# Kernel optimization log

Measured on AMD Instinct MI355X. Metric: run time of the kernel, lower is better.

Reference implementation:

```python
import jax, jax.numpy as jnp
import numpy as np

D_MODEL = 1024
NUM_HEADS = 16
D_K = D_MODEL // NUM_HEADS
LN_EPS = 1e-5


def setup_inputs() -> dict:
    key = jax.random.key(0)
    ks = jax.random.split(key, 13)
    B, S, D = 2, 2048, D_MODEL
    s = 1.0 / np.sqrt(D)
    return {
        "query": jax.random.normal(ks[0], (B, S, D), jnp.float32),
        "key": jax.random.normal(ks[1], (B, S, D), jnp.float32),
        "value": jax.random.normal(ks[2], (B, S, D), jnp.float32),
        "Wq": jax.random.normal(ks[3], (D, D), jnp.float32) * s,
        "bq": jnp.zeros((D,), jnp.float32),
        "Wk": jax.random.normal(ks[4], (D, D), jnp.float32) * s,
        "bk": jnp.zeros((D,), jnp.float32),
        "Wv": jax.random.normal(ks[5], (D, D), jnp.float32) * s,
        "bv": jnp.zeros((D,), jnp.float32),
        "Wo": jax.random.normal(ks[6], (D, D), jnp.float32) * s,
        "bo": jnp.zeros((D,), jnp.float32),
        "gamma": jnp.ones((D,), jnp.float32),
        "beta": jnp.zeros((D,), jnp.float32),
    }


def _mha(query, key, value, Wq, bq, Wk, bk, Wv, bv, Wo, bo, gamma, beta):
    B, S, D = query.shape
    H, dk = NUM_HEADS, D_K
    # projections (x @ W + b), reshape to [B, H, S, dk]
    Q = (query @ Wq + bq).reshape(B, S, H, dk).transpose(0, 2, 1, 3)
    K = (key @ Wk + bk).reshape(B, S, H, dk).transpose(0, 2, 1, 3)
    V = (value @ Wv + bv).reshape(B, S, H, dk).transpose(0, 2, 1, 3)
    scores = jnp.einsum("bhsd,bhtd->bhst", Q, K) / np.sqrt(dk).astype(np.float32)
    attn = jax.nn.softmax(scores, axis=-1)  # dropout is identity at inference
    ctx = jnp.einsum("bhst,bhtd->bhsd", attn, V)
    ctx = ctx.transpose(0, 2, 1, 3).reshape(B, S, D)
    out = ctx @ Wo + bo
    # residual + LayerNorm
    x = out + query
    mu = jnp.mean(x, axis=-1, keepdims=True)
    var = jnp.mean(jnp.square(x - mu), axis=-1, keepdims=True)
    y = (x - mu) / jnp.sqrt(var + LN_EPS) * gamma + beta
    return y, attn


def reference(query, key, value, Wq, bq, Wk, bk, Wv, bv, Wo, bo, gamma, beta):
    return _mha(query, key, value, Wq, bq, Wk, bk, Wv, bv, Wo, bo, gamma, beta)
```

## Files before the change

kernel.cpp:

```cpp
#include <hip/hip_runtime.h>
#include <stdint.h>

typedef __attribute__((ext_vector_type(8))) short bf16x8;
typedef __attribute__((ext_vector_type(4))) float f32x4;
typedef unsigned short u16;

#define DEVINL static __device__ __forceinline__

namespace {
constexpr int kS = 2048, kD = 1024, kH = 16, kDK = 64;
constexpr int kBS = 4096, kBH = 32;
constexpr float kEps = 1e-5f;
constexpr float kQScale = 0.125f * 1.44269504088896340736f;
}

DEVINL u16 f2bf(float f) {
  union { float f; unsigned u; } v; v.f = f;
  unsigned r = v.u + 0x7fffu + ((v.u >> 16) & 1u);
  return (u16)(r >> 16);
}
DEVINL unsigned pk2(float lo, float hi) {
  return (__float_as_uint(hi) & 0xffff0000u) | (__float_as_uint(lo) >> 16);
}
DEVINL f32x4 mfma16(bf16x8 a, bf16x8 b, f32x4 c) {
  return __builtin_amdgcn_mfma_f32_16x16x32_bf16(a, b, c, 0, 0, 0);
}

__global__ __launch_bounds__(256, 4)
void k_cvt_x(const float* __restrict__ xq, const float* __restrict__ xk,
             const float* __restrict__ xv, u16* __restrict__ oq,
             u16* __restrict__ ok, u16* __restrict__ ov) {
  const int z = blockIdx.y;
  const float* __restrict__ src = (z == 0) ? xq : (z == 1) ? xk : xv;
  u16* __restrict__ dst = (z == 0) ? oq : (z == 1) ? ok : ov;
  const size_t idx = (size_t)blockIdx.x * 256 + threadIdx.x;
  const float4 a = *reinterpret_cast<const float4*>(&src[idx * 8]);
  const float4 b = *reinterpret_cast<const float4*>(&src[idx * 8 + 4]);
  uint4 o;
  o.x = pk2(a.x, a.y); o.y = pk2(a.z, a.w);
  o.z = pk2(b.x, b.y); o.w = pk2(b.z, b.w);
  *reinterpret_cast<uint4*>(&dst[idx * 8]) = o;
}

__global__ __launch_bounds__(256, 4)
void k_cvt_w(const float* __restrict__ wq, const float* __restrict__ wk,
             const float* __restrict__ wv, const float* __restrict__ wo,
             u16* __restrict__ oq, u16* __restrict__ ok,
             u16* __restrict__ ov, u16* __restrict__ oo) {
  const int z = blockIdx.z;
  const float* __restrict__ W = (z == 0) ? wq : (z == 1) ? wk : (z == 2) ? wv : wo;
  u16* __restrict__ Wt = (z == 0) ? oq : (z == 1) ? ok : (z == 2) ? ov : oo;
  const int n0 = blockIdx.x * 64, k0 = blockIdx.y * 64;
  const int tid = threadIdx.x;
  __shared__ u16 Tl[64][65];
#pragma unroll
  for (int p = 0; p < 4; ++p) {
    const int idx = tid + p * 256;
    const int kr = idx >> 4, cg = (idx & 15) * 4;
    const float4 v = *reinterpret_cast<const float4*>(&W[(size_t)(k0 + kr) * kD + n0 + cg]);
    Tl[kr][cg + 0] = f2bf(v.x);
    Tl[kr][cg + 1] = f2bf(v.y);
    Tl[kr][cg + 2] = f2bf(v.z);
    Tl[kr][cg + 3] = f2bf(v.w);
  }
  __syncthreads();
  const int n = tid >> 2, kc = (tid & 3) * 16;
  u16 buf[16];
#pragma unroll
  for (int i = 0; i < 16; ++i) buf[i] = Tl[kc + i][n];
  *reinterpret_cast<bf16x8*>(&Wt[(size_t)(n0 + n) * kD + k0 + kc]) =
      *reinterpret_cast<const bf16x8*>(&buf[0]);
  *reinterpret_cast<bf16x8*>(&Wt[(size_t)(n0 + n) * kD + k0 + kc + 8]) =
      *reinterpret_cast<const bf16x8*>(&buf[8]);
}

__global__ __launch_bounds__(256, 2)
void k_proj(const u16* __restrict__ Xq, const u16* __restrict__ Xk,
            const u16* __restrict__ Xv, const u16* __restrict__ Wtq,
            const u16* __restrict__ Wtk, const u16* __restrict__ Wtv,
            const float* __restrict__ bq, const float* __restrict__ bk,
            const float* __restrict__ bv, u16* __restrict__ Qo,
            u16* __restrict__ Ko, u16* __restrict__ Vo) {
  const int which = blockIdx.z;
  const u16* __restrict__ X = (which == 0) ? Xq : (which == 1) ? Xk : Xv;
  const u16* __restrict__ Wt = (which == 0) ? Wtq : (which == 1) ? Wtk : Wtv;
  const float* __restrict__ bias = (which == 0) ? bq : (which == 1) ? bk : bv;

  const int n0 = blockIdx.x * 128, m0 = blockIdx.y * 128;
  const int tid = threadIdx.x, w = tid >> 6, l = tid & 63;
  const int l15 = l & 15, lh = l >> 4;

  __shared__ u16 Al[128][72];
  __shared__ u16 Bl[128][72];

  f32x4 acc[2][8];
#pragma unroll
  for (int i = 0; i < 2; ++i)
#pragma unroll
    for (int j = 0; j < 8; ++j) acc[i][j] = f32x4{0.f, 0.f, 0.f, 0.f};

  for (int k0 = 0; k0 < kD; k0 += 64) {
    __syncthreads();
#pragma unroll
    for (int p = 0; p < 4; ++p) {
      const int idx = tid + p * 256;
      const int row = idx >> 3, c = (idx & 7) * 8;
      *reinterpret_cast<bf16x8*>(&Al[row][c]) =
          *reinterpret_cast<const bf16x8*>(&X[(size_t)(m0 + row) * kD + k0 + c]);
      *reinterpret_cast<bf16x8*>(&Bl[row][c]) =
          *reinterpret_cast<const bf16x8*>(&Wt[(size_t)(n0 + row) * kD + k0 + c]);
    }
    __syncthreads();
#pragma unroll
    for (int kq = 0; kq < 2; ++kq) {
      const int kk = kq * 32 + lh * 8;
      bf16x8 a[2], b[8];
#pragma unroll
      for (int mi = 0; mi < 2; ++mi)
        a[mi] = *reinterpret_cast<const bf16x8*>(&Al[w * 32 + mi * 16 + l15][kk]);
#pragma unroll
      for (int nj = 0; nj < 8; ++nj)
        b[nj] = *reinterpret_cast<const bf16x8*>(&Bl[nj * 16 + l15][kk]);
      if (which == 2) {
#pragma unroll
        for (int mi = 0; mi < 2; ++mi)
#pragma unroll
          for (int nj = 0; nj < 8; ++nj)
            acc[mi][nj] = mfma16(a[mi], b[nj], acc[mi][nj]);
      } else {
#pragma unroll
        for (int mi = 0; mi < 2; ++mi)
#pragma unroll
          for (int nj = 0; nj < 8; ++nj)
            acc[mi][nj] = mfma16(b[nj], a[mi], acc[mi][nj]);
      }
    }
  }

  if (which == 2) {
#pragma unroll
    for (int mi = 0; mi < 2; ++mi)
#pragma unroll
      for (int nj = 0; nj < 8; ++nj) {
        const int col = n0 + nj * 16 + l15;
        const int h = col >> 6, d = col & 63;
        const float bvv = bias[col];
        const int row0 = m0 + w * 32 + mi * 16 + lh * 4;
        const int b_ = row0 >> 11, s0 = row0 & 2047;
        uint2 pkv;
        pkv.x = pk2(acc[mi][nj][0] + bvv, acc[mi][nj][1] + bvv);
        pkv.y = pk2(acc[mi][nj][2] + bvv, acc[mi][nj][3] + bvv);
        *reinterpret_cast<uint2*>(
            &Vo[((size_t)(b_ * kH + h) * kDK + d) * kS + s0]) = pkv;
      }
  } else {
    u16* __restrict__ Out = (which == 0) ? Qo : Ko;
    const float os = (which == 0) ? kQScale : 1.0f;
#pragma unroll
    for (int mi = 0; mi < 2; ++mi) {
      const int srow = m0 + w * 32 + mi * 16 + l15;
      const int b_ = srow >> 11, s_ = srow & 2047;
#pragma unroll
      for (int nj = 0; nj < 8; ++nj) {
        const int c0 = n0 + nj * 16 + lh * 4;
        const int h = c0 >> 6, d0 = c0 & 63;
        const float4 b4 = *reinterpret_cast<const float4*>(&bias[c0]);
        uint2 pkv;
        pkv.x = pk2((acc[mi][nj][0] + b4.x) * os, (acc[mi][nj][1] + b4.y) * os);
        pkv.y = pk2((acc[mi][nj][2] + b4.z) * os, (acc[mi][nj][3] + b4.w) * os);
        *reinterpret_cast<uint2*>(
            &Out[((size_t)(b_ * kH + h) * kS + s_) * kDK + d0]) = pkv;
      }
    }
  }
}

__global__ __launch_bounds__(256, 2)
void k_attn(const u16* __restrict__ Qw, const u16* __restrict__ Kw,
            const u16* __restrict__ Vtw, float* __restrict__ attn_out,
            u16* __restrict__ ctx_out) {
  const int q0 = blockIdx.x * 128;
  const int bh = blockIdx.y;
  const int tid = threadIdx.x, w = tid >> 6, l = tid & 63;
  const int l15 = l & 15, lh = l >> 4;

  __shared__ u16 PQs[128][72];
  __shared__ u16 Ksh[2][64][72];
  __shared__ u16 Vsh[2][64][72];

  const u16* __restrict__ Qg = Qw + ((size_t)bh * kS + q0) * kDK;
  const u16* __restrict__ Kg = Kw + (size_t)bh * kS * kDK;
  const u16* __restrict__ Vtg = Vtw + (size_t)bh * kDK * kS;

#pragma unroll
  for (int p = 0; p < 4; ++p) {
    const int idx = tid + p * 256;
    const int row = idx >> 3, c = (idx & 7) * 8;
    *reinterpret_cast<bf16x8*>(&PQs[row][c]) =
        *reinterpret_cast<const bf16x8*>(&Qg[(size_t)row * kDK + c]);
  }
  bf16x8 kreg[2], vreg[2];
#pragma unroll
  for (int p = 0; p < 2; ++p) {
    const int idx = tid + p * 256;
    const int row = idx >> 3, c = (idx & 7) * 8;
    kreg[p] = *reinterpret_cast<const bf16x8*>(&Kg[(size_t)row * kDK + c]);
  }
#pragma unroll
  for (int p = 0; p < 2; ++p) {
    const int idx = tid + p * 256;
    const int row = idx >> 3, c = (idx & 7) * 8;
    *reinterpret_cast<bf16x8*>(&Ksh[0][row][c]) = kreg[p];
  }
  __syncthreads();

  bf16x8 qf[2][2];
#pragma unroll
  for (int mi = 0; mi < 2; ++mi)
#pragma unroll
    for (int kq = 0; kq < 2; ++kq)
      qf[mi][kq] = *reinterpret_cast<const bf16x8*>(
          &PQs[w * 32 + mi * 16 + l15][kq * 32 + lh * 8]);

  float lsum[2] = {0.f, 0.f};
  for (int t = 0; t < 32; ++t) {
    const int buf = t & 1;
    if (t + 1 < 32) {
      const u16* __restrict__ src = Kg + (size_t)(t + 1) * 64 * kDK;
#pragma unroll
      for (int p = 0; p < 2; ++p) {
        const int idx = tid + p * 256;
        const int row = idx >> 3, c = (idx & 7) * 8;
        kreg[p] = *reinterpret_cast<const bf16x8*>(&src[(size_t)row * kDK + c]);
      }
    }
    f32x4 sacc[2][4];
#pragma unroll
    for (int mi = 0; mi < 2; ++mi)
#pragma unroll
      for (int nj = 0; nj < 4; ++nj) sacc[mi][nj] = f32x4{0.f, 0.f, 0.f, 0.f};
    __builtin_amdgcn_s_setprio(1);
#pragma unroll
    for (int kq = 0; kq < 2; ++kq) {
      const int kk = kq * 32 + lh * 8;
      bf16x8 kf[4];
#pragma unroll
      for (int nj = 0; nj < 4; ++nj)
        kf[nj] = *reinterpret_cast<const bf16x8*>(&Ksh[buf][nj * 16 + l15][kk]);
#pragma unroll
      for (int mi = 0; mi < 2; ++mi)
#pragma unroll
        for (int nj = 0; nj < 4; ++nj)
          sacc[mi][nj] = mfma16(kf[nj], qf[mi][kq], sacc[mi][nj]);
    }
    __builtin_amdgcn_s_setprio(0);
#pragma unroll
    for (int mi = 0; mi < 2; ++mi) {
      float s0 = 0.f;
#pragma unroll
      for (int nj = 0; nj < 4; ++nj)
#pragma unroll
        for (int r = 0; r < 4; ++r) s0 += exp2f(sacc[mi][nj][r]);
      lsum[mi] += s0;
    }
    if (t + 1 < 32) {
#pragma unroll
      for (int p = 0; p < 2; ++p) {
        const int idx = tid + p * 256;
        const int row = idx >> 3, c = (idx & 7) * 8;
        *reinterpret_cast<bf16x8*>(&Ksh[buf ^ 1][row][c]) = kreg[p];
      }
    }
    __syncthreads();
  }

  float lg[2];
#pragma unroll
  for (int mi = 0; mi < 2; ++mi) {
    float lv = lsum[mi];
    lv += __shfl_xor(lv, 16, 64);
    lv += __shfl_xor(lv, 32, 64);
    lg[mi] = -log2f(lv);
  }

  f32x4 oacc[2][4];
#pragma unroll
  for (int mi = 0; mi < 2; ++mi)
#pragma unroll
    for (int ni = 0; ni < 4; ++ni) oacc[mi][ni] = f32x4{0.f, 0.f, 0.f, 0.f};

  float* __restrict__ attn_base =
      attn_out + (size_t)bh * kS * kS + (size_t)q0 * kS;

#pragma unroll
  for (int p = 0; p < 2; ++p) {
    const int idx = tid + p * 256;
    const int row = idx >> 3, c = (idx & 7) * 8;
    kreg[p] = *reinterpret_cast<const bf16x8*>(&Kg[(size_t)row * kDK + c]);
    vreg[p] = *reinterpret_cast<const bf16x8*>(&Vtg[(size_t)row * kS + c]);
  }
#pragma unroll
  for (int p = 0; p < 2; ++p) {
    const int idx = tid + p * 256;
    const int row = idx >> 3, c = (idx & 7) * 8;
    *reinterpret_cast<bf16x8*>(&Ksh[0][row][c]) = kreg[p];
    *reinterpret_cast<bf16x8*>(&Vsh[0][row][c]) = vreg[p];
  }
  __syncthreads();

  for (int t = 0; t < 32; ++t) {
    const int buf = t & 1;
    const int t0 = t * 64;
    if (t + 1 < 32) {
      const u16* __restrict__ ksrc = Kg + (size_t)(t0 + 64) * kDK;
#pragma unroll
      for (int p = 0; p < 2; ++p) {
        const int idx = tid + p * 256;
        const int row = idx >> 3, c = (idx & 7) * 8;
        kreg[p] = *reinterpret_cast<const bf16x8*>(&ksrc[(size_t)row * kDK + c]);
        vreg[p] = *reinterpret_cast<const bf16x8*>(&Vtg[(size_t)row * kS + t0 + 64 + c]);
      }
    }
    f32x4 sacc[2][4];
#pragma unroll
    for (int mi = 0; mi < 2; ++mi)
#pragma unroll
      for (int nj = 0; nj < 4; ++nj) sacc[mi][nj] = f32x4{0.f, 0.f, 0.f, 0.f};
    __builtin_amdgcn_s_setprio(1);
#pragma unroll
    for (int kq = 0; kq < 2; ++kq) {
      const int kk = kq * 32 + lh * 8;
      bf16x8 kf[4];
#pragma unroll
      for (int nj = 0; nj < 4; ++nj)
        kf[nj] = *reinterpret_cast<const bf16x8*>(&Ksh[buf][nj * 16 + l15][kk]);
#pragma unroll
      for (int mi = 0; mi < 2; ++mi)
#pragma unroll
        for (int nj = 0; nj < 4; ++nj)
          sacc[mi][nj] = mfma16(kf[nj], qf[mi][kq], sacc[mi][nj]);
    }
    __builtin_amdgcn_s_setprio(0);
#pragma unroll
    for (int mi = 0; mi < 2; ++mi) {
      const int q = w * 32 + mi * 16 + l15;
      float* __restrict__ arow = attn_base + (size_t)q * kS + t0;
#pragma unroll
      for (int nj = 0; nj < 4; ++nj) {
        float4 pv;
        pv.x = exp2f(sacc[mi][nj][0] + lg[mi]);
        pv.y = exp2f(sacc[mi][nj][1] + lg[mi]);
        pv.z = exp2f(sacc[mi][nj][2] + lg[mi]);
        pv.w = exp2f(sacc[mi][nj][3] + lg[mi]);
        *reinterpret_cast<float4*>(&arow[nj * 16 + lh * 4]) = pv;
        uint2 pkv; pkv.x = pk2(pv.x, pv.y); pkv.y = pk2(pv.z, pv.w);
        *reinterpret_cast<uint2*>(&PQs[q][nj * 16 + lh * 4]) = pkv;
      }
    }
    __builtin_amdgcn_s_setprio(1);
#pragma unroll
    for (int kq = 0; kq < 2; ++kq) {
      const int kk = kq * 32 + lh * 8;
      bf16x8 pa[2], vb[4];
#pragma unroll
      for (int mi = 0; mi < 2; ++mi)
        pa[mi] = *reinterpret_cast<const bf16x8*>(&PQs[w * 32 + mi * 16 + l15][kk]);
#pragma unroll
      for (int ni = 0; ni < 4; ++ni)
        vb[ni] = *reinterpret_cast<const bf16x8*>(&Vsh[buf][ni * 16 + l15][kk]);
#pragma unroll
      for (int mi = 0; mi < 2; ++mi)
#pragma unroll
        for (int ni = 0; ni < 4; ++ni)
          oacc[mi][ni] = mfma16(vb[ni], pa[mi], oacc[mi][ni]);
    }
    __builtin_amdgcn_s_setprio(0);
    if (t + 1 < 32) {
#pragma unroll
      for (int p = 0; p < 2; ++p) {
        const int idx = tid + p * 256;
        const int row = idx >> 3, c = (idx & 7) * 8;
        *reinterpret_cast<bf16x8*>(&Ksh[buf ^ 1][row][c]) = kreg[p];
        *reinterpret_cast<bf16x8*>(&Vsh[buf ^ 1][row][c]) = vreg[p];
      }
    }
    __syncthreads();
  }

  const int b_ = bh >> 4, h = bh & 15;
#pragma unroll
  for (int mi = 0; mi < 2; ++mi) {
    const int s_ = q0 + w * 32 + mi * 16 + l15;
#pragma unroll
    for (int ni = 0; ni < 4; ++ni) {
      const int d0 = ni * 16 + lh * 4;
      uint2 pkv;
      pkv.x = pk2(oacc[mi][ni][0], oacc[mi][ni][1]);
      pkv.y = pk2(oacc[mi][ni][2], oacc[mi][ni][3]);
      *reinterpret_cast<uint2*>(
          &ctx_out[((size_t)(b_ * kS + s_)) * kD + h * kDK + d0]) = pkv;
    }
  }
}

__global__ __launch_bounds__(256, 2)
void k_oproj(const u16* __restrict__ Cw, const u16* __restrict__ Wto,
             const float* __restrict__ bo, const float* __restrict__ query,
             float* __restrict__ Xout) {
  const int n0 = blockIdx.x * 128, m0 = blockIdx.y * 128;
  const int tid = threadIdx.x, w = tid >> 6, l = tid & 63;
  const int l15 = l & 15, lh = l >> 4;

  __shared__ u16 Al[128][72];
  __shared__ u16 Bl[128][72];

  f32x4 acc[2][8];
#pragma unroll
  for (int i = 0; i < 2; ++i)
#pragma unroll
    for (int j = 0; j < 8; ++j) acc[i][j] = f32x4{0.f, 0.f, 0.f, 0.f};

  for (int k0 = 0; k0 < kD; k0 += 64) {
    __syncthreads();
#pragma unroll
    for (int p = 0; p < 4; ++p) {
      const int idx = tid + p * 256;
      const int row = idx >> 3, c = (idx & 7) * 8;
      *reinterpret_cast<bf16x8*>(&Al[row][c]) =
          *reinterpret_cast<const bf16x8*>(&Cw[(size_t)(m0 + row) * kD + k0 + c]);
      *reinterpret_cast<bf16x8*>(&Bl[row][c]) =
          *reinterpret_cast<const bf16x8*>(&Wto[(size_t)(n0 + row) * kD + k0 + c]);
    }
    __syncthreads();
#pragma unroll
    for (int kq = 0; kq < 2; ++kq) {
      const int kk = kq * 32 + lh * 8;
      bf16x8 a[2], b[8];
#pragma unroll
      for (int mi = 0; mi < 2; ++mi)
        a[mi] = *reinterpret_cast<const bf16x8*>(&Al[w * 32 + mi * 16 + l15][kk]);
#pragma unroll
      for (int nj = 0; nj < 8; ++nj)
        b[nj] = *reinterpret_cast<const bf16x8*>(&Bl[nj * 16 + l15][kk]);
#pragma unroll
      for (int mi = 0; mi < 2; ++mi)
#pragma unroll
        for (int nj = 0; nj < 8; ++nj)
          acc[mi][nj] = mfma16(b[nj], a[mi], acc[mi][nj]);
    }
  }

#pragma unroll
  for (int mi = 0; mi < 2; ++mi) {
    const int row = m0 + w * 32 + mi * 16 + l15;
#pragma unroll
    for (int nj = 0; nj < 8; ++nj) {
      const int c0 = n0 + nj * 16 + lh * 4;
      const float4 b4 = *reinterpret_cast<const float4*>(&bo[c0]);
      const float4 q4 = *reinterpret_cast<const float4*>(&query[(size_t)row * kD + c0]);
      float4 o;
      o.x = acc[mi][nj][0] + b4.x + q4.x;
      o.y = acc[mi][nj][1] + b4.y + q4.y;
      o.z = acc[mi][nj][2] + b4.z + q4.z;
      o.w = acc[mi][nj][3] + b4.w + q4.w;
      *reinterpret_cast<float4*>(&Xout[(size_t)row * kD + c0]) = o;
    }
  }
}

__global__ __launch_bounds__(256, 4)
void k_ln(float* __restrict__ Y, const float* __restrict__ gamma,
          const float* __restrict__ beta) {
  const int row = blockIdx.x;
  float* __restrict__ x = Y + (size_t)row * kD;
  const int tid = threadIdx.x;
  const float4 v = reinterpret_cast<const float4*>(x)[tid];
  float s = v.x + v.y + v.z + v.w;
  float sq = v.x * v.x + v.y * v.y + v.z * v.z + v.w * v.w;
#pragma unroll
  for (int mk = 1; mk < 64; mk <<= 1) {
    s += __shfl_xor(s, mk, 64);
    sq += __shfl_xor(sq, mk, 64);
  }
  __shared__ float ss[4], ssq[4];
  if ((tid & 63) == 0) { ss[tid >> 6] = s; ssq[tid >> 6] = sq; }
  __syncthreads();
  s = ss[0] + ss[1] + ss[2] + ss[3];
  sq = ssq[0] + ssq[1] + ssq[2] + ssq[3];
  const float mu = s * (1.f / kD);
  const float rstd = rsqrtf(sq * (1.f / kD) - mu * mu + kEps);
  const float4 g = reinterpret_cast<const float4*>(gamma)[tid];
  const float4 bb = reinterpret_cast<const float4*>(beta)[tid];
  float4 o;
  o.x = (v.x - mu) * rstd * g.x + bb.x;
  o.y = (v.y - mu) * rstd * g.y + bb.y;
  o.z = (v.z - mu) * rstd * g.z + bb.z;
  o.w = (v.w - mu) * rstd * g.w + bb.w;
  reinterpret_cast<float4*>(x)[tid] = o;
}

extern "C" void kernel_launch(void* const* d_in, const int* in_sizes, int n_in,
                              void* d_out, int out_size, void* d_ws, size_t ws_size,
                              hipStream_t stream) {
  (void)in_sizes; (void)n_in; (void)out_size; (void)ws_size;
  const float* query = (const float*)d_in[0];
  const float* key_i = (const float*)d_in[1];
  const float* value = (const float*)d_in[2];
  const float* Wq = (const float*)d_in[3];
  const float* bq = (const float*)d_in[4];
  const float* Wk = (const float*)d_in[5];
  const float* bk = (const float*)d_in[6];
  const float* Wv = (const float*)d_in[7];
  const float* bv = (const float*)d_in[8];
  const float* Wo = (const float*)d_in[9];
  const float* bo = (const float*)d_in[10];
  const float* gamma = (const float*)d_in[11];
  const float* beta = (const float*)d_in[12];

  float* y_out = (float*)d_out;
  float* attn_out = y_out + (size_t)kBS * kD;

  u16* Xbq = (u16*)d_ws;
  u16* Xbk = Xbq + (size_t)kBS * kD;
  u16* Xbv = Xbk + (size_t)kBS * kD;
  u16* Wtq = Xbv + (size_t)kBS * kD;
  u16* Wtk = Wtq + (size_t)kD * kD;
  u16* Wtv = Wtk + (size_t)kD * kD;
  u16* Wto = Wtv + (size_t)kD * kD;
  u16* Qw  = Wto + (size_t)kD * kD;
  u16* Kw  = Qw + (size_t)kBH * kS * kDK;
  u16* Vtw = Kw + (size_t)kBH * kS * kDK;
  u16* Cw  = Xbq;

  k_cvt_x<<<dim3(2048, 3), 256, 0, stream>>>(query, key_i, value, Xbq, Xbk, Xbv);
  k_cvt_w<<<dim3(16, 16, 4), 256, 0, stream>>>(Wq, Wk, Wv, Wo, Wtq, Wtk, Wtv, Wto);
  k_proj<<<dim3(kD / 128, kBS / 128, 3), 256, 0, stream>>>(
      Xbq, Xbk, Xbv, Wtq, Wtk, Wtv, bq, bk, bv, Qw, Kw, Vtw);
  k_attn<<<dim3(kS / 128, kBH), 256, 0, stream>>>(Qw, Kw, Vtw, attn_out, Cw);
  k_oproj<<<dim3(kD / 128, kBS / 128), 256, 0, stream>>>(Cw, Wto, bo, query, y_out);
  k_ln<<<dim3(kBS), 256, 0, stream>>>(y_out, gamma, beta);
}
```

Before: 316.1 us.

## Load GEMM tiles directly to LDS with XOR-swizzled layout in projections

The QKV and output projection GEMMs now use global_load_lds (16-byte direct global-to-LDS copies) instead of staging tiles through registers. The LDS tiles drop their padding and use an XOR swizzle on 8-element k-chunks to avoid bank conflicts. Occupancy hints rise from 2 to 3 blocks per CU, which the smaller LDS footprint allows. This aims to cut register pressure and VGPR round trips during tile loads, but the correctness of the swizzle and the direct-to-LDS addressing depends on the per-wave LDS base layout.

```diff
diff --git a/kernel.cpp b/kernel.cpp
--- a/kernel.cpp
+++ b/kernel.cpp
@@ -25,6 +25,12 @@
 DEVINL f32x4 mfma16(bf16x8 a, bf16x8 b, f32x4 c) {
   return __builtin_amdgcn_mfma_f32_16x16x32_bf16(a, b, c, 0, 0, 0);
 }
+DEVINL void gl_lds16(const u16* g, u16* l) {
+  __builtin_amdgcn_global_load_lds(
+      (const __attribute__((address_space(1))) void*)(g),
+      (__attribute__((address_space(3))) void*)(l), 16, 0, 0);
+}
+DEVINL int kswz(int kq, int lh, int aswz) { return (((kq << 2) + lh) ^ aswz) << 3; }
 
 __global__ __launch_bounds__(256, 4)
 void k_cvt_x(const float* __restrict__ xq, const float* __restrict__ xk,
@@ -74,7 +80,7 @@
       *reinterpret_cast<const bf16x8*>(&buf[8]);
 }
 
-__global__ __launch_bounds__(256, 2)
+__global__ __launch_bounds__(256, 3)
 void k_proj(const u16* __restrict__ Xq, const u16* __restrict__ Xk,
             const u16* __restrict__ Xv, const u16* __restrict__ Wtq,
             const u16* __restrict__ Wtk, const u16* __restrict__ Wtv,
@@ -89,9 +95,10 @@
   const int n0 = blockIdx.x * 128, m0 = blockIdx.y * 128;
   const int tid = threadIdx.x, w = tid >> 6, l = tid & 63;
   const int l15 = l & 15, lh = l >> 4;
-
-  __shared__ u16 Al[128][72];
-  __shared__ u16 Bl[128][72];
+  const int aswz = l15 & 7;
+
+  __shared__ u16 Al[128][64];
+  __shared__ u16 Bl[128][64];
 
   f32x4 acc[2][8];
 #pragma unroll
@@ -103,17 +110,18 @@
     __syncthreads();
 #pragma unroll
     for (int p = 0; p < 4; ++p) {
-      const int idx = tid + p * 256;
-      const int row = idx >> 3, c = (idx & 7) * 8;
-      *reinterpret_cast<bf16x8*>(&Al[row][c]) =
-          *reinterpret_cast<const bf16x8*>(&X[(size_t)(m0 + row) * kD + k0 + c]);
-      *reinterpret_cast<bf16x8*>(&Bl[row][c]) =
-          *reinterpret_cast<const bf16x8*>(&Wt[(size_t)(n0 + row) * kD + k0 + c]);
+      const int slot = p * 256 + tid;
+      const int row = slot >> 3;
+      const int k8 = (slot & 7) ^ (row & 7);
+      gl_lds16(&X[(size_t)(m0 + row) * kD + k0 + k8 * 8],
+               &Al[0][0] + (size_t)(p * 256 + w * 64) * 8);
+      gl_lds16(&Wt[(size_t)(n0 + row) * kD + k0 + k8 * 8],
+               &Bl[0][0] + (size_t)(p * 256 + w * 64) * 8);
     }
     __syncthreads();
 #pragma unroll
     for (int kq = 0; kq < 2; ++kq) {
-      const int kk = kq * 32 + lh * 8;
+      const int kk = kswz(kq, lh, aswz);
       bf16x8 a[2], b[8];
 #pragma unroll
       for (int mi = 0; mi < 2; ++mi)
@@ -403,16 +411,17 @@
   }
 }
 
-__global__ __launch_bounds__(256, 2)
+__global__ __launch_bounds__(256, 3)
 void k_oproj(const u16* __restrict__ Cw, const u16* __restrict__ Wto,
              const float* __restrict__ bo, const float* __restrict__ query,
              float* __restrict__ Xout) {
   const int n0 = blockIdx.x * 128, m0 = blockIdx.y * 128;
   const int tid = threadIdx.x, w = tid >> 6, l = tid & 63;
   const int l15 = l & 15, lh = l >> 4;
-
-  __shared__ u16 Al[128][72];
-  __shared__ u16 Bl[128][72];
+  const int aswz = l15 & 7;
+
+  __shared__ u16 Al[128][64];
+  __shared__ u16 Bl[128][64];
 
   f32x4 acc[2][8];
 #pragma unroll
@@ -424,17 +433,18 @@
     __syncthreads();
 #pragma unroll
     for (int p = 0; p < 4; ++p) {
-      const int idx = tid + p * 256;
-      const int row = idx >> 3, c = (idx & 7) * 8;
-      *reinterpret_cast<bf16x8*>(&Al[row][c]) =
-          *reinterpret_cast<const bf16x8*>(&Cw[(size_t)(m0 + row) * kD + k0 + c]);
-      *reinterpret_cast<bf16x8*>(&Bl[row][c]) =
-          *reinterpret_cast<const bf16x8*>(&Wto[(size_t)(n0 + row) * kD + k0 + c]);
+      const int slot = p * 256 + tid;
+      const int row = slot >> 3;
+      const int k8 = (slot & 7) ^ (row & 7);
+      gl_lds16(&Cw[(size_t)(m0 + row) * kD + k0 + k8 * 8],
+               &Al[0][0] + (size_t)(p * 256 + w * 64) * 8);
+      gl_lds16(&Wto[(size_t)(n0 + row) * kD + k0 + k8 * 8],
+               &Bl[0][0] + (size_t)(p * 256 + w * 64) * 8);
     }
     __syncthreads();
 #pragma unroll
     for (int kq = 0; kq < 2; ++kq) {
-      const int kk = kq * 32 + lh * 8;
+      const int kk = kswz(kq, lh, aswz);
       bf16x8 a[2], b[8];
 #pragma unroll
       for (int mi = 0; mi < 2; ++mi)
```

Result: slower. 368.5 us (+16.6%).

## Double-buffer GEMM tiles via register prefetch and remap block grid orders

Applied to the files above, without the earlier changes.

The projection and output-projection GEMMs now prefetch the next K tile into registers while computing on the current LDS buffer. The tile is then written into a second LDS buffer, so each iteration needs one barrier instead of two, and MFMA sections get raised wave priority. The GEMM grids are transposed so consecutive blocks walk along M, and the attention grid is flattened with a custom mapping that interleaves heads across consecutive blocks. The aim is to hide global load latency and improve cache and scheduling locality, at the cost of double the LDS per block, which may reduce occupancy.

```diff
diff --git a/kernel.cpp b/kernel.cpp
--- a/kernel.cpp
+++ b/kernel.cpp
@@ -86,12 +86,12 @@
   const u16* __restrict__ Wt = (which == 0) ? Wtq : (which == 1) ? Wtk : Wtv;
   const float* __restrict__ bias = (which == 0) ? bq : (which == 1) ? bk : bv;
 
-  const int n0 = blockIdx.x * 128, m0 = blockIdx.y * 128;
+  const int m0 = blockIdx.x * 128, n0 = blockIdx.y * 128;
   const int tid = threadIdx.x, w = tid >> 6, l = tid & 63;
   const int l15 = l & 15, lh = l >> 4;
 
-  __shared__ u16 Al[128][72];
-  __shared__ u16 Bl[128][72];
+  __shared__ u16 Al[2][128][72];
+  __shared__ u16 Bl[2][128][72];
 
   f32x4 acc[2][8];
 #pragma unroll
@@ -99,28 +99,46 @@
 #pragma unroll
     for (int j = 0; j < 8; ++j) acc[i][j] = f32x4{0.f, 0.f, 0.f, 0.f};
 
-  for (int k0 = 0; k0 < kD; k0 += 64) {
-    __syncthreads();
-#pragma unroll
-    for (int p = 0; p < 4; ++p) {
-      const int idx = tid + p * 256;
-      const int row = idx >> 3, c = (idx & 7) * 8;
-      *reinterpret_cast<bf16x8*>(&Al[row][c]) =
-          *reinterpret_cast<const bf16x8*>(&X[(size_t)(m0 + row) * kD + k0 + c]);
-      *reinterpret_cast<bf16x8*>(&Bl[row][c]) =
-          *reinterpret_cast<const bf16x8*>(&Wt[(size_t)(n0 + row) * kD + k0 + c]);
-    }
-    __syncthreads();
+  bf16x8 xreg[4], wreg[4];
+#pragma unroll
+  for (int p = 0; p < 4; ++p) {
+    const int idx = tid + p * 256;
+    const int row = idx >> 3, c = (idx & 7) * 8;
+    xreg[p] = *reinterpret_cast<const bf16x8*>(&X[(size_t)(m0 + row) * kD + c]);
+    wreg[p] = *reinterpret_cast<const bf16x8*>(&Wt[(size_t)(n0 + row) * kD + c]);
+  }
+#pragma unroll
+  for (int p = 0; p < 4; ++p) {
+    const int idx = tid + p * 256;
+    const int row = idx >> 3, c = (idx & 7) * 8;
+    *reinterpret_cast<bf16x8*>(&Al[0][row][c]) = xreg[p];
+    *reinterpret_cast<bf16x8*>(&Bl[0][row][c]) = wreg[p];
+  }
+  __syncthreads();
+
+  for (int t = 0; t < 16; ++t) {
+    const int buf = t & 1;
+    if (t + 1 < 16) {
+      const int k0 = (t + 1) * 64;
+#pragma unroll
+      for (int p = 0; p < 4; ++p) {
+        const int idx = tid + p * 256;
+        const int row = idx >> 3, c = (idx & 7) * 8;
+        xreg[p] = *reinterpret_cast<const bf16x8*>(&X[(size_t)(m0 + row) * kD + k0 + c]);
+        wreg[p] = *reinterpret_cast<const bf16x8*>(&Wt[(size_t)(n0 + row) * kD + k0 + c]);
+      }
+    }
+    __builtin_amdgcn_s_setprio(1);
 #pragma unroll
     for (int kq = 0; kq < 2; ++kq) {
       const int kk = kq * 32 + lh * 8;
       bf16x8 a[2], b[8];
 #pragma unroll
       for (int mi = 0; mi < 2; ++mi)
-        a[mi] = *reinterpret_cast<const bf16x8*>(&Al[w * 32 + mi * 16 + l15][kk]);
+        a[mi] = *reinterpret_cast<const bf16x8*>(&Al[buf][w * 32 + mi * 16 + l15][kk]);
 #pragma unroll
       for (int nj = 0; nj < 8; ++nj)
-        b[nj] = *reinterpret_cast<const bf16x8*>(&Bl[nj * 16 + l15][kk]);
+        b[nj] = *reinterpret_cast<const bf16x8*>(&Bl[buf][nj * 16 + l15][kk]);
       if (which == 2) {
 #pragma unroll
         for (int mi = 0; mi < 2; ++mi)
@@ -135,6 +153,17 @@
             acc[mi][nj] = mfma16(b[nj], a[mi], acc[mi][nj]);
       }
     }
+    __builtin_amdgcn_s_setprio(0);
+    if (t + 1 < 16) {
+#pragma unroll
+      for (int p = 0; p < 4; ++p) {
+        const int idx = tid + p * 256;
+        const int row = idx >> 3, c = (idx & 7) * 8;
+        *reinterpret_cast<bf16x8*>(&Al[buf ^ 1][row][c]) = xreg[p];
+        *reinterpret_cast<bf16x8*>(&Bl[buf ^ 1][row][c]) = wreg[p];
+      }
+    }
+    __syncthreads();
   }
 
   if (which == 2) {
@@ -179,8 +208,9 @@
 void k_attn(const u16* __restrict__ Qw, const u16* __restrict__ Kw,
             const u16* __restrict__ Vtw, float* __restrict__ attn_out,
             u16* __restrict__ ctx_out) {
-  const int q0 = blockIdx.x * 128;
-  const int bh = blockIdx.y;
+  const int id = blockIdx.x;
+  const int bh = (id & 7) * 4 + ((id >> 3) & 3);
+  const int q0 = (id >> 5) * 128;
   const int tid = threadIdx.x, w = tid >> 6, l = tid & 63;
   const int l15 = l & 15, lh = l >> 4;
 
@@ -407,12 +437,12 @@
 void k_oproj(const u16* __restrict__ Cw, const u16* __restrict__ Wto,
              const float* __restrict__ bo, const float* __restrict__ query,
              float* __restrict__ Xout) {
-  const int n0 = blockIdx.x * 128, m0 = blockIdx.y * 128;
+  const int m0 = blockIdx.x * 128, n0 = blockIdx.y * 128;
   const int tid = threadIdx.x, w = tid >> 6, l = tid & 63;
   const int l15 = l & 15, lh = l >> 4;
 
-  __shared__ u16 Al[128][72];
-  __shared__ u16 Bl[128][72];
+  __shared__ u16 Al[2][128][72];
+  __shared__ u16 Bl[2][128][72];
 
   f32x4 acc[2][8];
 #pragma unroll
@@ -420,34 +450,63 @@
 #pragma unroll
     for (int j = 0; j < 8; ++j) acc[i][j] = f32x4{0.f, 0.f, 0.f, 0.f};
 
-  for (int k0 = 0; k0 < kD; k0 += 64) {
-    __syncthreads();
-#pragma unroll
-    for (int p = 0; p < 4; ++p) {
-      const int idx = tid + p * 256;
-      const int row = idx >> 3, c = (idx & 7) * 8;
-      *reinterpret_cast<bf16x8*>(&Al[row][c]) =
-          *reinterpret_cast<const bf16x8*>(&Cw[(size_t)(m0 + row) * kD + k0 + c]);
-      *reinterpret_cast<bf16x8*>(&Bl[row][c]) =
-          *reinterpret_cast<const bf16x8*>(&Wto[(size_t)(n0 + row) * kD + k0 + c]);
-    }
-    __syncthreads();
+  bf16x8 xreg[4], wreg[4];
+#pragma unroll
+  for (int p = 0; p < 4; ++p) {
+    const int idx = tid + p * 256;
+    const int row = idx >> 3, c = (idx & 7) * 8;
+    xreg[p] = *reinterpret_cast<const bf16x8*>(&Cw[(size_t)(m0 + row) * kD + c]);
+    wreg[p] = *reinterpret_cast<const bf16x8*>(&Wto[(size_t)(n0 + row) * kD + c]);
+  }
+#pragma unroll
+  for (int p = 0; p < 4; ++p) {
+    const int idx = tid + p * 256;
+    const int row = idx >> 3, c = (idx & 7) * 8;
+    *reinterpret_cast<bf16x8*>(&Al[0][row][c]) = xreg[p];
+    *reinterpret_cast<bf16x8*>(&Bl[0][row][c]) = wreg[p];
+  }
+  __syncthreads();
+
+  for (int t = 0; t < 16; ++t) {
+    const int buf = t & 1;
+    if (t + 1 < 16) {
+      const int k0 = (t + 1) * 64;
+#pragma unroll
+      for (int p = 0; p < 4; ++p) {
+        const int idx = tid + p * 256;
+        const int row = idx >> 3, c = (idx & 7) * 8;
+        xreg[p] = *reinterpret_cast<const bf16x8*>(&Cw[(size_t)(m0 + row) * kD + k0 + c]);
+        wreg[p] = *reinterpret_cast<const bf16x8*>(&Wto[(size_t)(n0 + row) * kD + k0 + c]);
+      }
+    }
+    __builtin_amdgcn_s_setprio(1);
 #pragma unroll
     for (int kq = 0; kq < 2; ++kq) {
       const int kk = kq * 32 + lh * 8;
       bf16x8 a[2], b[8];
 #pragma unroll
       for (int mi = 0; mi < 2; ++mi)
-        a[mi] = *reinterpret_cast<const bf16x8*>(&Al[w * 32 + mi * 16 + l15][kk]);
+        a[mi] = *reinterpret_cast<const bf16x8*>(&Al[buf][w * 32 + mi * 16 + l15][kk]);
 #pragma unroll
       for (int nj = 0; nj < 8; ++nj)
-        b[nj] = *reinterpret_cast<const bf16x8*>(&Bl[nj * 16 + l15][kk]);
+        b[nj] = *reinterpret_cast<const bf16x8*>(&Bl[buf][nj * 16 + l15][kk]);
 #pragma unroll
       for (int mi = 0; mi < 2; ++mi)
 #pragma unroll
         for (int nj = 0; nj < 8; ++nj)
           acc[mi][nj] = mfma16(b[nj], a[mi], acc[mi][nj]);
     }
+    __builtin_amdgcn_s_setprio(0);
+    if (t + 1 < 16) {
+#pragma unroll
+      for (int p = 0; p < 4; ++p) {
+        const int idx = tid + p * 256;
+        const int row = idx >> 3, c = (idx & 7) * 8;
+        *reinterpret_cast<bf16x8*>(&Al[buf ^ 1][row][c]) = xreg[p];
+        *reinterpret_cast<bf16x8*>(&Bl[buf ^ 1][row][c]) = wreg[p];
+      }
+    }
+    __syncthreads();
   }
 
 #pragma unroll
@@ -534,9 +593,9 @@
 
   k_cvt_x<<<dim3(2048, 3), 256, 0, stream>>>(query, key_i, value, Xbq, Xbk, Xbv);
   k_cvt_w<<<dim3(16, 16, 4), 256, 0, stream>>>(Wq, Wk, Wv, Wo, Wtq, Wtk, Wtv, Wto);
-  k_proj<<<dim3(kD / 128, kBS / 128, 3), 256, 0, stream>>>(
+  k_proj<<<dim3(kBS / 128, kD / 128, 3), 256, 0, stream>>>(
       Xbq, Xbk, Xbv, Wtq, Wtk, Wtv, bq, bk, bv, Qw, Kw, Vtw);
-  k_attn<<<dim3(kS / 128, kBH), 256, 0, stream>>>(Qw, Kw, Vtw, attn_out, Cw);
-  k_oproj<<<dim3(kD / 128, kBS / 128), 256, 0, stream>>>(Cw, Wto, bo, query, y_out);
+  k_attn<<<dim3(512), 256, 0, stream>>>(Qw, Kw, Vtw, attn_out, Cw);
+  k_oproj<<<dim3(kBS / 128, kD / 128), 256, 0, stream>>>(Cw, Wto, bo, query, y_out);
   k_ln<<<dim3(kBS), 256, 0, stream>>>(y_out, gamma, beta);
 }
```

Result: slower. 331.4 us (+4.8%).

## Single-buffer K/V shared tiles and raise attention kernel occupancy to 4 blocks

Applied to the files above, without the earlier changes.

Replaces the double-buffered K and V shared-memory tiles with single buffers, still prefetching the next tile into registers, and adds an extra barrier before each shared-memory overwrite. LDS per block drops from about 55 KB to about 37 KB, and launch bounds rise from 2 to 4 blocks per CU to hide latency with more resident waves. The cost is a second __syncthreads per iteration and a tighter register budget, which may cause spills. The per-thread load mapping is also changed to two contiguous 16-byte chunks per row.

```diff
diff --git a/kernel.cpp b/kernel.cpp
--- a/kernel.cpp
+++ b/kernel.cpp
@@ -175,7 +175,7 @@
   }
 }
 
-__global__ __launch_bounds__(256, 2)
+__global__ __launch_bounds__(256, 4)
 void k_attn(const u16* __restrict__ Qw, const u16* __restrict__ Kw,
             const u16* __restrict__ Vtw, float* __restrict__ attn_out,
             u16* __restrict__ ctx_out) {
@@ -185,12 +185,14 @@
   const int l15 = l & 15, lh = l >> 4;
 
   __shared__ u16 PQs[128][72];
-  __shared__ u16 Ksh[2][64][72];
-  __shared__ u16 Vsh[2][64][72];
+  __shared__ u16 Ksh[64][72];
+  __shared__ u16 Vsh[64][72];
 
   const u16* __restrict__ Qg = Qw + ((size_t)bh * kS + q0) * kDK;
   const u16* __restrict__ Kg = Kw + (size_t)bh * kS * kDK;
   const u16* __restrict__ Vtg = Vtw + (size_t)bh * kDK * kS;
+
+  const int srow = tid >> 2, sc = (tid & 3) * 16;
 
 #pragma unroll
   for (int p = 0; p < 4; ++p) {
@@ -199,18 +201,11 @@
     *reinterpret_cast<bf16x8*>(&PQs[row][c]) =
         *reinterpret_cast<const bf16x8*>(&Qg[(size_t)row * kDK + c]);
   }
-  bf16x8 kreg[2], vreg[2];
-#pragma unroll
-  for (int p = 0; p < 2; ++p) {
-    const int idx = tid + p * 256;
-    const int row = idx >> 3, c = (idx & 7) * 8;
-    kreg[p] = *reinterpret_cast<const bf16x8*>(&Kg[(size_t)row * kDK + c]);
-  }
-#pragma unroll
-  for (int p = 0; p < 2; ++p) {
-    const int idx = tid + p * 256;
-    const int row = idx >> 3, c = (idx & 7) * 8;
-    *reinterpret_cast<bf16x8*>(&Ksh[0][row][c]) = kreg[p];
+  {
+    const bf16x8 k0a = *reinterpret_cast<const bf16x8*>(&Kg[(size_t)srow * kDK + sc]);
+    const bf16x8 k0b = *reinterpret_cast<const bf16x8*>(&Kg[(size_t)srow * kDK + sc + 8]);
+    *reinterpret_cast<bf16x8*>(&Ksh[srow][sc]) = k0a;
+    *reinterpret_cast<bf16x8*>(&Ksh[srow][sc + 8]) = k0b;
   }
   __syncthreads();
 
@@ -222,17 +217,13 @@
       qf[mi][kq] = *reinterpret_cast<const bf16x8*>(
           &PQs[w * 32 + mi * 16 + l15][kq * 32 + lh * 8]);
 
+  bf16x8 kra, krb, vra, vrb;
   float lsum[2] = {0.f, 0.f};
   for (int t = 0; t < 32; ++t) {
-    const int buf = t & 1;
     if (t + 1 < 32) {
       const u16* __restrict__ src = Kg + (size_t)(t + 1) * 64 * kDK;
-#pragma unroll
-      for (int p = 0; p < 2; ++p) {
-        const int idx = tid + p * 256;
-        const int row = idx >> 3, c = (idx & 7) * 8;
-        kreg[p] = *reinterpret_cast<const bf16x8*>(&src[(size_t)row * kDK + c]);
-      }
+      kra = *reinterpret_cast<const bf16x8*>(&src[(size_t)srow * kDK + sc]);
+      krb = *reinterpret_cast<const bf16x8*>(&src[(size_t)srow * kDK + sc + 8]);
     }
     f32x4 sacc[2][4];
 #pragma unroll
@@ -246,7 +237,7 @@
       bf16x8 kf[4];
 #pragma unroll
       for (int nj = 0; nj < 4; ++nj)
-        kf[nj] = *reinterpret_cast<const bf16x8*>(&Ksh[buf][nj * 16 + l15][kk]);
+        kf[nj] = *reinterpret_cast<const bf16x8*>(&Ksh[nj * 16 + l15][kk]);
 #pragma unroll
       for (int mi = 0; mi < 2; ++mi)
 #pragma unroll
@@ -263,13 +254,10 @@
         for (int r = 0; r < 4; ++r) s0 += exp2f(sacc[mi][nj][r]);
       lsum[mi] += s0;
     }
+    __syncthreads();
     if (t + 1 < 32) {
-#pragma unroll
-      for (int p = 0; p < 2; ++p) {
-        const int idx = tid + p * 256;
-        const int row = idx >> 3, c = (idx & 7) * 8;
-        *reinterpret_cast<bf16x8*>(&Ksh[buf ^ 1][row][c]) = kreg[p];
-      }
+      *reinterpret_cast<bf16x8*>(&Ksh[srow][sc]) = kra;
+      *reinterpret_cast<bf16x8*>(&Ksh[srow][sc + 8]) = krb;
     }
     __syncthreads();
   }
@@ -292,34 +280,26 @@
   float* __restrict__ attn_base =
       attn_out + (size_t)bh * kS * kS + (size_t)q0 * kS;
 
-#pragma unroll
-  for (int p = 0; p < 2; ++p) {
-    const int idx = tid + p * 256;
-    const int row = idx >> 3, c = (idx & 7) * 8;
-    kreg[p] = *reinterpret_cast<const bf16x8*>(&Kg[(size_t)row * kDK + c]);
-    vreg[p] = *reinterpret_cast<const bf16x8*>(&Vtg[(size_t)row * kS + c]);
-  }
-#pragma unroll
-  for (int p = 0; p < 2; ++p) {
-    const int idx = tid + p * 256;
-    const int row = idx >> 3, c = (idx & 7) * 8;
-    *reinterpret_cast<bf16x8*>(&Ksh[0][row][c]) = kreg[p];
-    *reinterpret_cast<bf16x8*>(&Vsh[0][row][c]) = vreg[p];
+  {
+    const bf16x8 k0a = *reinterpret_cast<const bf16x8*>(&Kg[(size_t)srow * kDK + sc]);
+    const bf16x8 k0b = *reinterpret_cast<const bf16x8*>(&Kg[(size_t)srow * kDK + sc + 8]);
+    const bf16x8 v0a = *reinterpret_cast<const bf16x8*>(&Vtg[(size_t)srow * kS + sc]);
+    const bf16x8 v0b = *reinterpret_cast<const bf16x8*>(&Vtg[(size_t)srow * kS + sc + 8]);
+    *reinterpret_cast<bf16x8*>(&Ksh[srow][sc]) = k0a;
+    *reinterpret_cast<bf16x8*>(&Ksh[srow][sc + 8]) = k0b;
+    *reinterpret_cast<bf16x8*>(&Vsh[srow][sc]) = v0a;
+    *reinterpret_cast<bf16x8*>(&Vsh[srow][sc + 8]) = v0b;
   }
   __syncthreads();
 
   for (int t = 0; t < 32; ++t) {
-    const int buf = t & 1;
     const int t0 = t * 64;
     if (t + 1 < 32) {
       const u16* __restrict__ ksrc = Kg + (size_t)(t0 + 64) * kDK;
-#pragma unroll
-      for (int p = 0; p < 2; ++p) {
-        const int idx = tid + p * 256;
-        const int row = idx >> 3, c = (idx & 7) * 8;
-        kreg[p] = *reinterpret_cast<const bf16x8*>(&ksrc[(size_t)row * kDK + c]);
-        vreg[p] = *reinterpret_cast<const bf16x8*>(&Vtg[(size_t)row * kS + t0 + 64 + c]);
-      }
+      kra = *reinterpret_cast<const bf16x8*>(&ksrc[(size_t)srow * kDK + sc]);
+      krb = *reinterpret_cast<const bf16x8*>(&ksrc[(size_t)srow * kDK + sc + 8]);
+      vra = *reinterpret_cast<const bf16x8*>(&Vtg[(size_t)srow * kS + t0 + 64 + sc]);
+      vrb = *reinterpret_cast<const bf16x8*>(&Vtg[(size_t)srow * kS + t0 + 64 + sc + 8]);
     }
     f32x4 sacc[2][4];
 #pragma unroll
@@ -333,7 +313,7 @@
       bf16x8 kf[4];
 #pragma unroll
       for (int nj = 0; nj < 4; ++nj)
-        kf[nj] = *reinterpret_cast<const bf16x8*>(&Ksh[buf][nj * 16 + l15][kk]);
+        kf[nj] = *reinterpret_cast<const bf16x8*>(&Ksh[nj * 16 + l15][kk]);
 #pragma unroll
       for (int mi = 0; mi < 2; ++mi)
 #pragma unroll
@@ -367,7 +347,7 @@
         pa[mi] = *reinterpret_cast<const bf16x8*>(&PQs[w * 32 + mi * 16 + l15][kk]);
 #pragma unroll
       for (int ni = 0; ni < 4; ++ni)
-        vb[ni] = *reinterpret_cast<const bf16x8*>(&Vsh[buf][ni * 16 + l15][kk]);
+        vb[ni] = *reinterpret_cast<const bf16x8*>(&Vsh[ni * 16 + l15][kk]);
 #pragma unroll
       for (int mi = 0; mi < 2; ++mi)
 #pragma unroll
@@ -375,14 +355,12 @@
           oacc[mi][ni] = mfma16(vb[ni], pa[mi], oacc[mi][ni]);
     }
     __builtin_amdgcn_s_setprio(0);
+    __syncthreads();
     if (t + 1 < 32) {
-#pragma unroll
-      for (int p = 0; p < 2; ++p) {
-        const int idx = tid + p * 256;
-        const int row = idx >> 3, c = (idx & 7) * 8;
-        *reinterpret_cast<bf16x8*>(&Ksh[buf ^ 1][row][c]) = kreg[p];
-        *reinterpret_cast<bf16x8*>(&Vsh[buf ^ 1][row][c]) = vreg[p];
-      }
+      *reinterpret_cast<bf16x8*>(&Ksh[srow][sc]) = kra;
+      *reinterpret_cast<bf16x8*>(&Ksh[srow][sc + 8]) = krb;
+      *reinterpret_cast<bf16x8*>(&Vsh[srow][sc]) = vra;
+      *reinterpret_cast<bf16x8*>(&Vsh[srow][sc + 8]) = vrb;
     }
     __syncthreads();
   }
```

Result: slower. 408.2 us (+29.1%).
